# Performance work log

Measured on AMD Instinct MI355X. Metric: run time of the kernel, lower is better.

## Reference

```python
import jax, jax.numpy as jnp
import numpy as np

N = 10000
E = 320000
DIM_IN, DIM_H, DIM_OUT, HEADS = 256, 64, 32, 8
NEG_SLOPE = 0.2


def setup_inputs() -> dict:
    key = jax.random.key(0)
    ks = jax.random.split(key, 10)
    x = jax.random.normal(ks[0], (N, DIM_IN), dtype=jnp.float32)
    edge_index = jax.random.randint(ks[1], (2, E), 0, N, dtype=jnp.int64)
    def glorot(k, shape, fan_in):
        return jax.random.normal(k, shape, dtype=jnp.float32) / np.sqrt(fan_in)
    # layer 1: GATv2Conv(256 -> 64, heads=8)
    W1l = glorot(ks[2], (DIM_IN, HEADS * DIM_H), DIM_IN)
    W1r = glorot(ks[3], (DIM_IN, HEADS * DIM_H), DIM_IN)
    att1 = glorot(ks[4], (HEADS, DIM_H), DIM_H)
    b1 = jnp.zeros((HEADS * DIM_H,), dtype=jnp.float32)
    # layer 2: GATv2Conv(512 -> 32, heads=1)
    W2l = glorot(ks[5], (HEADS * DIM_H, DIM_OUT), HEADS * DIM_H)
    W2r = glorot(ks[6], (HEADS * DIM_H, DIM_OUT), HEADS * DIM_H)
    att2 = glorot(ks[7], (1, DIM_OUT), DIM_OUT)
    b2 = jnp.zeros((DIM_OUT,), dtype=jnp.float32)
    return {"x": x, "edge_index": edge_index, "W1l": W1l, "W1r": W1r,
            "att1": att1, "b1": b1, "W2l": W2l, "W2r": W2r, "att2": att2, "b2": b2}


def gatv2_conv(x, src, dst, Wl, Wr, att, bias, heads, out_ch, concat):
    n = x.shape[0]
    xl = (x @ Wl).reshape(n, heads, out_ch)  # source transform
    xr = (x @ Wr).reshape(n, heads, out_ch)  # target transform
    e = jax.nn.leaky_relu(xl[src] + xr[dst], NEG_SLOPE)       # [E,H,C]
    alpha = jnp.einsum('ehc,hc->eh', e, att)                  # [E,H]
    amax = jax.lax.stop_gradient(
        jax.ops.segment_max(alpha, dst, num_segments=n))      # [N,H]
    ex = jnp.exp(alpha - amax[dst])
    denom = jax.ops.segment_sum(ex, dst, num_segments=n)
    alpha = ex / (denom[dst] + 1e-16)
    msg = xl[src] * alpha[..., None]                          # [E,H,C]
    out = jax.ops.segment_sum(msg, dst, num_segments=n)       # [N,H,C]
    out = out.reshape(n, heads * out_ch) if concat else out.mean(axis=1)
    return out + bias


def reference(x, edge_index, W1l, W1r, att1, b1, W2l, W2r, att2, b2):
    n = x.shape[0]
    loops = jnp.arange(n, dtype=edge_index.dtype)
    src = jnp.concatenate([edge_index[0], loops])  # add_self_loops=True (PyG default)
    dst = jnp.concatenate([edge_index[1], loops])
    h = gatv2_conv(x, src, dst, W1l, W1r, att1, b1, HEADS, DIM_H, True)
    h = jax.nn.elu(h)
    h = gatv2_conv(h, src, dst, W2l, W2r, att2, b2, 1, DIM_OUT, True)
    return jax.nn.log_softmax(h, axis=1)
```

## Files before the change

kernel.cpp:

```cpp
#include <hip/hip_runtime.h>
#include <hip/hip_bf16.h>


constexpr int N_NODES = 10000;
constexpr int N_EDGES = 320000;
constexpr int ET      = N_EDGES + N_NODES;
constexpr float NEG_SLOPE = 0.2f;

constexpr int NB_COUNT  = (ET + 255) / 256;
constexpr int NB_CONVX  = (N_NODES * 64) / 256;
constexpr int NB_CONVW  = (1024 * 64) / 256;
constexpr int NB_CONVW2 = (64 * 128) / 256;
constexpr int NB_M1     = 79 * 8;

typedef __attribute__((ext_vector_type(8))) short short8;
typedef __attribute__((ext_vector_type(8))) unsigned short ushort8_t;
typedef __attribute__((ext_vector_type(4))) float floatx4;
typedef __attribute__((ext_vector_type(2))) float floatx2;

__device__ __forceinline__ float lrelu(float a) {
    return fmaxf(a, NEG_SLOPE * a);
}
__device__ __forceinline__ unsigned short f2bf(float f) {
    unsigned u = __float_as_uint(f);
    unsigned r = u + 0x7FFFu + ((u >> 16) & 1u);
    return (unsigned short)(r >> 16);
}
__device__ __forceinline__ float bf2f(unsigned short h) {
    return __uint_as_float((unsigned)h << 16);
}
__device__ __forceinline__ floatx2 pk_add(floatx2 a, floatx2 b) {
    floatx2 d;
    asm("v_pk_add_f32 %0, %1, %2" : "=v"(d) : "v"(a), "v"(b));
    return d;
}
__device__ __forceinline__ floatx2 pk_fma(floatx2 a, floatx2 b, floatx2 c) {
    floatx2 d;
    asm("v_pk_fma_f32 %0, %1, %2, %3" : "=v"(d) : "v"(a), "v"(b), "v"(c));
    return d;
}
__device__ __forceinline__ floatx2 unpk(unsigned w) {
    floatx2 r;
    r.x = __uint_as_float(w << 16);
    r.y = __uint_as_float(w & 0xffff0000u);
    return r;
}
__device__ __forceinline__ float red8_dpp(float p) {
    int x;
    x = __builtin_amdgcn_update_dpp(0, __float_as_int(p), 0xB1, 0xF, 0xF, true);
    p += __int_as_float(x);
    x = __builtin_amdgcn_update_dpp(0, __float_as_int(p), 0x4E, 0xF, 0xF, true);
    p += __int_as_float(x);
    x = __builtin_amdgcn_update_dpp(0, __float_as_int(p), 0x141, 0xF, 0xF, true);
    p += __int_as_float(x);
    return p;
}
__device__ __forceinline__ float red8max_dpp(float p) {
    int x;
    x = __builtin_amdgcn_update_dpp(0, __float_as_int(p), 0xB1, 0xF, 0xF, true);
    p = fmaxf(p, __int_as_float(x));
    x = __builtin_amdgcn_update_dpp(0, __float_as_int(p), 0x4E, 0xF, 0xF, true);
    p = fmaxf(p, __int_as_float(x));
    x = __builtin_amdgcn_update_dpp(0, __float_as_int(p), 0x141, 0xF, 0xF, true);
    p = fmaxf(p, __int_as_float(x));
    return p;
}
__device__ __forceinline__ float ror8_add(float p) {
    int x = __builtin_amdgcn_update_dpp(0, __float_as_int(p), 0x128, 0xF, 0xF, true);
    return p + __int_as_float(x);
}


__global__ __launch_bounds__(256) void k_prep(const int* __restrict__ ei,
        int* __restrict__ deg, const float* __restrict__ x,
        unsigned short* __restrict__ A, const float* __restrict__ Wl,
        const float* __restrict__ Wr, unsigned short* __restrict__ Bt,
        const float* __restrict__ W2l, const float* __restrict__ W2r,
        unsigned short* __restrict__ Bt2) {
    int b = blockIdx.x, t = threadIdx.x;
    if (b < NB_COUNT) {
        int e = b * 256 + t;
        if (e >= ET) return;
        int d = (e < N_EDGES) ? ei[N_EDGES + e] : (e - N_EDGES);
        atomicAdd(&deg[d], 1);
    } else if (b < NB_COUNT + NB_CONVX) {
        int idx = (b - NB_COUNT) * 256 + t;
        int m = idx >> 6, kg = (idx & 63) << 2;
        float4 v = *reinterpret_cast<const float4*>(x + (size_t)m * 256 + kg);
        ushort4 hi = make_ushort4(f2bf(v.x), f2bf(v.y), f2bf(v.z), f2bf(v.w));
        *reinterpret_cast<ushort4*>(A + (size_t)m * 256 + kg) = hi;
    } else if (b < NB_COUNT + NB_CONVX + NB_CONVW) {
        int idx = (b - NB_COUNT - NB_CONVX) * 256 + t;
        int n = idx >> 6, kg = (idx & 63) << 2;
        const float* src = (n < 512) ? (Wl + n) : (Wr + (n - 512));
        float v0 = src[(size_t)(kg + 0) * 512];
        float v1 = src[(size_t)(kg + 1) * 512];
        float v2 = src[(size_t)(kg + 2) * 512];
        float v3 = src[(size_t)(kg + 3) * 512];
        ushort4 hi = make_ushort4(f2bf(v0), f2bf(v1), f2bf(v2), f2bf(v3));
        *reinterpret_cast<ushort4*>(Bt + (size_t)n * 256 + kg) = hi;
    } else {
        int idx = (b - NB_COUNT - NB_CONVX - NB_CONVW) * 256 + t;
        int j = idx >> 7, kg = (idx & 127) << 2;
        const float* src = (j < 32) ? (W2l + j) : (W2r + (j - 32));
        float v0 = src[(size_t)(kg + 0) * 32];
        float v1 = src[(size_t)(kg + 1) * 32];
        float v2 = src[(size_t)(kg + 2) * 32];
        float v3 = src[(size_t)(kg + 3) * 32];
        ushort4 hi = make_ushort4(f2bf(v0), f2bf(v1), f2bf(v2), f2bf(v3));
        *reinterpret_cast<ushort4*>(Bt2 + (size_t)j * 512 + kg) = hi;
    }
}


__global__ __launch_bounds__(1024) void k_scan(const int* __restrict__ deg,
                                               int* __restrict__ offs) {
    __shared__ int part[1024];
    const int CH = 10;
    int t = threadIdx.x;
    int base = t * CH;
    int loc[CH];
    int s = 0;
    for (int i = 0; i < CH; ++i) {
        int idx = base + i;
        int v = (idx < N_NODES) ? deg[idx] : 0;
        loc[i] = s; s += v;
    }
    part[t] = s;
    __syncthreads();
    for (int o = 1; o < 1024; o <<= 1) {
        int add = (t >= o) ? part[t - o] : 0;
        __syncthreads();
        part[t] += add;
        __syncthreads();
    }
    int excl = part[t] - s;
    for (int i = 0; i < CH; ++i) {
        int idx = base + i;
        if (idx < N_NODES) offs[idx] = excl + loc[i];
    }
    if (t == 1023) offs[N_NODES] = part[1023];
}


__global__ __launch_bounds__(256) void k_scm1(const int* __restrict__ ei,
        const int* __restrict__ offs, int* __restrict__ deg,
        int* __restrict__ ssrc, const unsigned short* __restrict__ A,
        const unsigned short* __restrict__ Bt, unsigned short* __restrict__ xl1b,
        unsigned short* __restrict__ xr1b) {
    __shared__ unsigned short As[128 * 40];
    __shared__ unsigned short Bs[128 * 40];
    int t = threadIdx.x;
    if (blockIdx.x < NB_COUNT) {
        int e = blockIdx.x * 256 + t;
        if (e >= ET) return;
        int s, d;
        if (e < N_EDGES) { s = ei[e]; d = ei[N_EDGES + e]; }
        else             { s = d = e - N_EDGES; }
        int pos = offs[d] + atomicAdd(&deg[d], -1) - 1;
        ssrc[pos] = s;
        return;
    }
    int bb = blockIdx.x - NB_COUNT;
    int row0 = (bb % 79) * 128, n0 = (bb / 79) * 128;
    int wave = t >> 6, L = t & 63;
    int wm = wave & 1, wn = wave >> 1;
    int q = L >> 4, rr = L & 15;
    floatx4 acc[4][4];
#pragma unroll
    for (int i = 0; i < 4; ++i)
#pragma unroll
        for (int j = 0; j < 4; ++j) acc[i][j] = (floatx4){0.f, 0.f, 0.f, 0.f};
    int ra = t >> 2,        ka = (t & 3) * 8;
    int rb = (t + 256) >> 2, kb = ((t + 256) & 3) * 8;
    int gma = row0 + ra; gma = (gma < N_NODES) ? gma : (N_NODES - 1);
    int gmb = row0 + rb; gmb = (gmb < N_NODES) ? gmb : (N_NODES - 1);
    for (int kc = 0; kc < 256; kc += 32) {
        __syncthreads();
        *reinterpret_cast<uint4*>(&As[ra * 40 + ka]) =
            *reinterpret_cast<const uint4*>(A + (size_t)gma * 256 + kc + ka);
        *reinterpret_cast<uint4*>(&As[rb * 40 + kb]) =
            *reinterpret_cast<const uint4*>(A + (size_t)gmb * 256 + kc + kb);
        *reinterpret_cast<uint4*>(&Bs[ra * 40 + ka]) =
            *reinterpret_cast<const uint4*>(Bt + (size_t)(n0 + ra) * 256 + kc + ka);
        *reinterpret_cast<uint4*>(&Bs[rb * 40 + kb]) =
            *reinterpret_cast<const uint4*>(Bt + (size_t)(n0 + rb) * 256 + kc + kb);
        __syncthreads();
        short8 af[4], bf[4];
#pragma unroll
        for (int st = 0; st < 4; ++st)
            af[st] = *reinterpret_cast<const short8*>(
                &As[(wm * 64 + st * 16 + rr) * 40 + q * 8]);
#pragma unroll
        for (int st = 0; st < 4; ++st)
            bf[st] = *reinterpret_cast<const short8*>(
                &Bs[(wn * 64 + st * 16 + rr) * 40 + q * 8]);
#pragma unroll
        for (int i = 0; i < 4; ++i)
#pragma unroll
            for (int j = 0; j < 4; ++j)
                acc[i][j] = __builtin_amdgcn_mfma_f32_16x16x32_bf16(
                    af[i], bf[j], acc[i][j], 0, 0, 0);
    }
#pragma unroll
    for (int j = 0; j < 4; ++j) {
        int gc = n0 + wn * 64 + j * 16 + rr;
        unsigned short* dst = (gc < 512) ? xl1b : xr1b;
        int col = (gc < 512) ? gc : (gc - 512);
#pragma unroll
        for (int i = 0; i < 4; ++i)
#pragma unroll
            for (int r = 0; r < 4; ++r) {
                int gr = row0 + wm * 64 + i * 16 + q * 4 + r;
                if (gr < N_NODES)
                    dst[(size_t)gr * 512 + col] = f2bf(acc[i][j][r]);
            }
    }
}

__global__ __launch_bounds__(256) void k_node1f(const int* __restrict__ offs,
        const int* __restrict__ ssrc, const unsigned short* __restrict__ xl1b,
        const unsigned short* __restrict__ xr1b, const float* __restrict__ att1,
        const float* __restrict__ b1, unsigned short* __restrict__ h1b) {
    __shared__ float comb[2][64][9];
    int t = threadIdx.x;
    int wave = t >> 6, lane = t & 63;
    int ni = wave >> 1, wv = wave & 1;
    int n = blockIdx.x * 2 + ni;
    int beg0 = offs[n], d = offs[n + 1] - beg0;
    int half = (d + 1) >> 1;
    int beg = beg0 + (wv ? half : 0);
    int dcnt = wv ? (d - half) : half;
    floatx2 xrp0, xrp1, xrp2, xrp3;
    floatx2 c1p0, c1p1, c1p2, c1p3;
    floatx2 c2p0, c2p1, c2p2, c2p3;
    float K0;
    {
        ushort8_t xru = *reinterpret_cast<const ushort8_t*>(
            xr1b + (size_t)n * 512 + lane * 8);
        union { ushort8_t v; uint4 w; } cv; cv.v = xru;
        xrp0 = unpk(cv.w.x); xrp1 = unpk(cv.w.y);
        xrp2 = unpk(cv.w.z); xrp3 = unpk(cv.w.w);
        const float* atrow = att1 + lane * 8;
        float4 c0 = *reinterpret_cast<const float4*>(atrow);
        float4 c1 = *reinterpret_cast<const float4*>(atrow + 4);
        c1p0 = (floatx2){0.6f * c0.x, 0.6f * c0.y};
        c1p1 = (floatx2){0.6f * c0.z, 0.6f * c0.w};
        c1p2 = (floatx2){0.6f * c1.x, 0.6f * c1.y};
        c1p3 = (floatx2){0.6f * c1.z, 0.6f * c1.w};
        c2p0 = (floatx2){0.4f * c0.x, 0.4f * c0.y};
        c2p1 = (floatx2){0.4f * c0.z, 0.4f * c0.w};
        c2p2 = (floatx2){0.4f * c1.x, 0.4f * c1.y};
        c2p3 = (floatx2){0.4f * c1.z, 0.4f * c1.w};
        K0 = c1p0.x * xrp0.x + c1p0.y * xrp0.y
           + c1p1.x * xrp1.x + c1p1.y * xrp1.y
           + c1p2.x * xrp2.x + c1p2.y * xrp2.y
           + c1p3.x * xrp3.x + c1p3.y * xrp3.y;
    }
    floatx2 k0p = (floatx2){K0, 0.f};
    float l = 0.f;
    floatx2 ac0 = {0.f, 0.f}, ac1 = {0.f, 0.f}, ac2 = {0.f, 0.f}, ac3 = {0.f, 0.f};
    const int* sp = ssrc + beg;
    const char* xlbase = reinterpret_cast<const char*>(xl1b) + lane * 16;
    auto ld_row = [&](int off) -> ushort8_t {
        return *reinterpret_cast<const ushort8_t*>(xlbase + off);
    };
    for (int b0 = 0; b0 < dcnt; b0 += 64) {
        int bn = dcnt - b0; if (bn > 64) bn = 64;
        int idxv = sp[b0 + ((lane < bn) ? lane : (bn - 1))];
        auto off_at = [&](int k) -> int {
            int kc = (k < bn) ? k : (bn - 1);
            return __shfl(idxv, kc, 64) << 10;
        };
        auto edge = [&](ushort8_t u, int idx) {
            union { ushort8_t v; uint4 w; } cv; cv.v = u;
            floatx2 xs0 = unpk(cv.w.x), xs1 = unpk(cv.w.y),
                    xs2 = unpk(cv.w.z), xs3 = unpk(cv.w.w);
            floatx2 dd = pk_fma(xs0, c1p0, k0p);
            dd = pk_fma(xs1, c1p1, dd);
            dd = pk_fma(xs2, c1p2, dd);
            dd = pk_fma(xs3, c1p3, dd);
            floatx2 a0 = pk_add(xs0, xrp0);
            floatx2 a1 = pk_add(xs1, xrp1);
            floatx2 a2 = pk_add(xs2, xrp2);
            floatx2 a3 = pk_add(xs3, xrp3);
            a0.x = fabsf(a0.x); a0.y = fabsf(a0.y);
            a1.x = fabsf(a1.x); a1.y = fabsf(a1.y);
            a2.x = fabsf(a2.x); a2.y = fabsf(a2.y);
            a3.x = fabsf(a3.x); a3.y = fabsf(a3.y);
            dd = pk_fma(a0, c2p0, dd);
            dd = pk_fma(a1, c2p1, dd);
            dd = pk_fma(a2, c2p2, dd);
            dd = pk_fma(a3, c2p3, dd);
            float p = red8_dpp(dd.x + dd.y);
            float w = __expf(fminf(p, 60.f));
            if (idx >= bn) w = 0.f;
            l += w;
            floatx2 wp = (floatx2){w, w};
            ac0 = pk_fma(xs0, wp, ac0);
            ac1 = pk_fma(xs1, wp, ac1);
            ac2 = pk_fma(xs2, wp, ac2);
            ac3 = pk_fma(xs3, wp, ac3);
        };
        ushort8_t u0 = ld_row(off_at(0));
        ushort8_t u1 = ld_row(off_at(1));
        ushort8_t u2 = ld_row(off_at(2));
        ushort8_t u3 = ld_row(off_at(3));
        for (int i = 0; i < bn; i += 4) {
            ushort8_t p0 = ld_row(off_at(i + 4));
            ushort8_t p1 = ld_row(off_at(i + 5));
            ushort8_t p2 = ld_row(off_at(i + 6));
            ushort8_t p3 = ld_row(off_at(i + 7));
            edge(u0, i);
            edge(u1, i + 1);
            edge(u2, i + 2);
            edge(u3, i + 3);
            u0 = p0; u1 = p1; u2 = p2; u3 = p3;
        }
    }
    if (wv == 1) {
        float* cb = &comb[ni][lane][0];
        cb[0] = ac0.x; cb[1] = ac0.y; cb[2] = ac1.x; cb[3] = ac1.y;
        cb[4] = ac2.x; cb[5] = ac2.y; cb[6] = ac3.x; cb[7] = ac3.y;
        cb[8] = l;
    }
    __syncthreads();
    if (wv == 0) {
        const float* cb = &comb[ni][lane][0];
        float av0 = ac0.x + cb[0], av1 = ac0.y + cb[1];
        float av2 = ac1.x + cb[2], av3 = ac1.y + cb[3];
        float av4 = ac2.x + cb[4], av5 = ac2.y + cb[5];
        float av6 = ac3.x + cb[6], av7 = ac3.y + cb[7];
        float lt = l + cb[8];
        float inv = 1.f / (lt + 1e-16f);
        const float* brow = b1 + lane * 8;
        float av[8] = {av0, av1, av2, av3, av4, av5, av6, av7};
        ushort8_t vout;
#pragma unroll
        for (int j = 0; j < 8; ++j) {
            float v = av[j] * inv + brow[j];
            v = (v > 0.f) ? v : (__expf(v) - 1.f);
            vout[j] = f2bf(v);
        }
        *reinterpret_cast<ushort8_t*>(h1b + (size_t)n * 512 + lane * 8) = vout;
    }
}


__global__ __launch_bounds__(256) void k_mfma2(const unsigned short* __restrict__ h1b,
        const unsigned short* __restrict__ Bt2, float* __restrict__ xw2) {
    __shared__ unsigned short Hs[64 * 40];
    __shared__ unsigned short Ws[64 * 40];
    int t = threadIdx.x;
    int wave = t >> 6, L = t & 63;
    int row0 = blockIdx.x * 64;
    int q = L >> 4, rr = L & 15;
    floatx4 acc[4];
#pragma unroll
    for (int j = 0; j < 4; ++j) acc[j] = (floatx4){0.f, 0.f, 0.f, 0.f};
    int ra = t >> 2, ka = (t & 3) * 8;
    int gma = row0 + ra; gma = (gma < N_NODES) ? gma : (N_NODES - 1);
    for (int kc = 0; kc < 512; kc += 32) {
        __syncthreads();
        *reinterpret_cast<uint4*>(&Hs[ra * 40 + ka]) =
            *reinterpret_cast<const uint4*>(h1b + (size_t)gma * 512 + kc + ka);
        *reinterpret_cast<uint4*>(&Ws[ra * 40 + ka]) =
            *reinterpret_cast<const uint4*>(Bt2 + (size_t)ra * 512 + kc + ka);
        __syncthreads();
        short8 af = *reinterpret_cast<const short8*>(
            &Hs[(wave * 16 + rr) * 40 + q * 8]);
#pragma unroll
        for (int j = 0; j < 4; ++j) {
            short8 bf = *reinterpret_cast<const short8*>(
                &Ws[(j * 16 + rr) * 40 + q * 8]);
            acc[j] = __builtin_amdgcn_mfma_f32_16x16x32_bf16(af, bf, acc[j], 0, 0, 0);
        }
    }
#pragma unroll
    for (int j = 0; j < 4; ++j) {
        int gc = j * 16 + rr;
#pragma unroll
        for (int r = 0; r < 4; ++r) {
            int gr = row0 + wave * 16 + q * 4 + r;
            if (gr < N_NODES) xw2[(size_t)gr * 64 + gc] = acc[j][r];
        }
    }
}

__global__ __launch_bounds__(256) void k_node2f(const int* __restrict__ offs,
        const int* __restrict__ ssrc, const float* __restrict__ xw2,
        const float* __restrict__ att2, const float* __restrict__ b2,
        float* __restrict__ out) {
    int t = threadIdx.x;
    int wave = t >> 6, lane = t & 63;
    int n = blockIdx.x * 4 + wave;
    if (n >= N_NODES) return;
    int ej = lane >> 3;
    int cg = lane & 7;
    int beg = offs[n], dcnt = offs[n + 1] - beg;
    float4 xr = *reinterpret_cast<const float4*>(
                    xw2 + (size_t)n * 64 + 32 + cg * 4);
    float4 at = *reinterpret_cast<const float4*>(att2 + cg * 4);
    float l = 0.f;
    float4 ac = {0.f, 0.f, 0.f, 0.f};
    const int* sp = ssrc + beg;
    const char* xwbase = reinterpret_cast<const char*>(xw2) + cg * 16;
    auto ld_row = [&](int off) -> float4 {
        return *reinterpret_cast<const float4*>(xwbase + off);
    };
    for (int b0 = 0; b0 < dcnt; b0 += 64) {
        int bn = dcnt - b0; if (bn > 64) bn = 64;
        int idxv = sp[b0 + ((lane < bn) ? lane : (bn - 1))];
        auto off_at = [&](int k) -> int {
            int kc = (k < bn) ? k : (bn - 1);
            return __shfl(idxv, kc, 64) << 8;
        };
        float4 uA  = ld_row(off_at(ej));
        float4 uB  = ld_row(off_at(8 + ej));
        float4 uA1 = ld_row(off_at(16 + ej));
        float4 uB1 = ld_row(off_at(24 + ej));
        for (int base = 0; base < bn; base += 16) {
            float4 uA2 = ld_row(off_at(base + 32 + ej));
            float4 uB2 = ld_row(off_at(base + 40 + ej));
            float pA0 = lrelu(uA.x + xr.x) * at.x + lrelu(uA.z + xr.z) * at.z;
            float pA1 = lrelu(uA.y + xr.y) * at.y + lrelu(uA.w + xr.w) * at.w;
            float pB0 = lrelu(uB.x + xr.x) * at.x + lrelu(uB.z + xr.z) * at.z;
            float pB1 = lrelu(uB.y + xr.y) * at.y + lrelu(uB.w + xr.w) * at.w;
            float pA = red8_dpp(pA0 + pA1);
            float pB = red8_dpp(pB0 + pB1);
            if (base + ej >= bn)     pA = -1e30f;
            if (base + 8 + ej >= bn) pB = -1e30f;
            float wA = __expf(fminf(pA, 60.f));
            float wB = __expf(fminf(pB, 60.f));
            l += wA + wB;
            ac.x += wA * uA.x + wB * uB.x;
            ac.y += wA * uA.y + wB * uB.y;
            ac.z += wA * uA.z + wB * uB.z;
            ac.w += wA * uA.w + wB * uB.w;
            uA = uA1; uB = uB1; uA1 = uA2; uB1 = uB2;
        }
    }
    l = ror8_add(l); l += __shfl_xor(l, 16); l += __shfl_xor(l, 32);
    ac.x = ror8_add(ac.x); ac.x += __shfl_xor(ac.x, 16); ac.x += __shfl_xor(ac.x, 32);
    ac.y = ror8_add(ac.y); ac.y += __shfl_xor(ac.y, 16); ac.y += __shfl_xor(ac.y, 32);
    ac.z = ror8_add(ac.z); ac.z += __shfl_xor(ac.z, 16); ac.z += __shfl_xor(ac.z, 32);
    ac.w = ror8_add(ac.w); ac.w += __shfl_xor(ac.w, 16); ac.w += __shfl_xor(ac.w, 32);
    float inv = 1.f / (l + 1e-16f);
    float4 bb = *reinterpret_cast<const float4*>(b2 + cg * 4);
    float4 v;
    v.x = ac.x * inv + bb.x; v.y = ac.y * inv + bb.y;
    v.z = ac.z * inv + bb.z; v.w = ac.w * inv + bb.w;
    float mx = red8max_dpp(fmaxf(fmaxf(v.x, v.y), fmaxf(v.z, v.w)));
    float se = red8_dpp(__expf(v.x - mx) + __expf(v.y - mx)
                      + __expf(v.z - mx) + __expf(v.w - mx));
    float ls = __logf(se);
    v.x = v.x - mx - ls; v.y = v.y - mx - ls;
    v.z = v.z - mx - ls; v.w = v.w - mx - ls;
    if (ej == 0)
        *reinterpret_cast<float4*>(out + (size_t)n * 32 + cg * 4) = v;
}


extern "C" void kernel_launch(void* const* d_in, const int* in_sizes, int n_in,
                              void* d_out, int out_size, void* d_ws, size_t ws_size,
                              hipStream_t stream) {
    (void)in_sizes; (void)n_in; (void)out_size; (void)ws_size;
    const float* x    = (const float*)d_in[0];
    const int*   ei   = (const int*)d_in[1];
    const float* W1l  = (const float*)d_in[2];
    const float* W1r  = (const float*)d_in[3];
    const float* att1 = (const float*)d_in[4];
    const float* b1   = (const float*)d_in[5];
    const float* W2l  = (const float*)d_in[6];
    const float* W2r  = (const float*)d_in[7];
    const float* att2 = (const float*)d_in[8];
    const float* b2   = (const float*)d_in[9];
    float* outp = (float*)d_out;

    char* ws = (char*)d_ws;
    size_t o = 0;
    auto alloc = [&](size_t bytes) {
        char* p = ws + o;
        o = (o + bytes + 255) & ~(size_t)255;
        return p;
    };
    unsigned short* xl1b = (unsigned short*)alloc((size_t)N_NODES * 512 * 2);
    unsigned short* xr1b = (unsigned short*)alloc((size_t)N_NODES * 512 * 2);
    unsigned short* h1b  = (unsigned short*)alloc((size_t)N_NODES * 512 * 2);
    float* xw2    = (float*)alloc((size_t)N_NODES * 64 * 4);
    unsigned short* Abf = (unsigned short*)alloc((size_t)N_NODES * 256 * 2);
    unsigned short* Bbf = (unsigned short*)alloc((size_t)1024 * 256 * 2);
    unsigned short* Bt2 = (unsigned short*)alloc((size_t)64 * 512 * 2);
    int*   deg    = (int*)alloc((size_t)N_NODES * 4);
    int*   offs   = (int*)alloc((size_t)(N_NODES + 1) * 4);
    int*   ssrc   = (int*)alloc((size_t)ET * 4);

    hipMemsetAsync(deg, 0, (size_t)N_NODES * 4, stream);

    k_prep   <<<NB_COUNT + NB_CONVX + NB_CONVW + NB_CONVW2, 256, 0, stream>>>(
                 ei, deg, x, Abf, W1l, W1r, Bbf, W2l, W2r, Bt2);
    k_scan   <<<1,                    1024, 0, stream>>>(deg, offs);
    k_scm1   <<<NB_COUNT + NB_M1,      256, 0, stream>>>(ei, offs, deg, ssrc,
                                                         Abf, Bbf, xl1b, xr1b);
    k_node1f <<<N_NODES / 2,           256, 0, stream>>>(offs, ssrc, xl1b, xr1b, att1, b1, h1b);
    k_mfma2  <<<(N_NODES + 63) / 64,   256, 0, stream>>>(h1b, Bt2, xw2);
    k_node2f <<<(N_NODES + 3) / 4,     256, 0, stream>>>(offs, ssrc, xw2, att2, b2, outp);
}
```

Before: 201.9 us.

## Assign one wave per node in layer-1 aggregation with deeper prefetch

Each wave now processes a whole node's edge list alone, so two waves no longer split a node and merge partial sums through shared memory with a block barrier. To keep enough gathers in flight, the edge loop is unrolled to eight rows with two prefetch groups. A launch-bounds occupancy hint is also added. This removes the LDS merge and __syncthreads, but each wave's serial chain doubles in length and the larger register footprint could reduce occupancy.

```diff
diff --git a/kernel.cpp b/kernel.cpp
--- a/kernel.cpp
+++ b/kernel.cpp
@@ -218,19 +218,15 @@
     }
 }
 
-__global__ __launch_bounds__(256) void k_node1f(const int* __restrict__ offs,
+__global__ __launch_bounds__(256, 4) void k_node1f(const int* __restrict__ offs,
         const int* __restrict__ ssrc, const unsigned short* __restrict__ xl1b,
         const unsigned short* __restrict__ xr1b, const float* __restrict__ att1,
         const float* __restrict__ b1, unsigned short* __restrict__ h1b) {
-    __shared__ float comb[2][64][9];
     int t = threadIdx.x;
     int wave = t >> 6, lane = t & 63;
-    int ni = wave >> 1, wv = wave & 1;
-    int n = blockIdx.x * 2 + ni;
-    int beg0 = offs[n], d = offs[n + 1] - beg0;
-    int half = (d + 1) >> 1;
-    int beg = beg0 + (wv ? half : 0);
-    int dcnt = wv ? (d - half) : half;
+    int n = blockIdx.x * 4 + wave;
+    if (n >= N_NODES) return;
+    int beg = offs[n], dcnt = offs[n + 1] - beg;
     floatx2 xrp0, xrp1, xrp2, xrp3;
     floatx2 c1p0, c1p1, c1p2, c1p3;
     floatx2 c2p0, c2p1, c2p2, c2p3;
@@ -302,48 +298,46 @@
             ac2 = pk_fma(xs2, wp, ac2);
             ac3 = pk_fma(xs3, wp, ac3);
         };
-        ushort8_t u0 = ld_row(off_at(0));
-        ushort8_t u1 = ld_row(off_at(1));
-        ushort8_t u2 = ld_row(off_at(2));
-        ushort8_t u3 = ld_row(off_at(3));
-        for (int i = 0; i < bn; i += 4) {
-            ushort8_t p0 = ld_row(off_at(i + 4));
-            ushort8_t p1 = ld_row(off_at(i + 5));
-            ushort8_t p2 = ld_row(off_at(i + 6));
-            ushort8_t p3 = ld_row(off_at(i + 7));
-            edge(u0, i);
-            edge(u1, i + 1);
-            edge(u2, i + 2);
-            edge(u3, i + 3);
-            u0 = p0; u1 = p1; u2 = p2; u3 = p3;
+        ushort8_t uA0 = ld_row(off_at(0));
+        ushort8_t uA1 = ld_row(off_at(1));
+        ushort8_t uA2 = ld_row(off_at(2));
+        ushort8_t uA3 = ld_row(off_at(3));
+        ushort8_t uB0 = ld_row(off_at(4));
+        ushort8_t uB1 = ld_row(off_at(5));
+        ushort8_t uB2 = ld_row(off_at(6));
+        ushort8_t uB3 = ld_row(off_at(7));
+        for (int i = 0; i < bn; i += 8) {
+            ushort8_t pA0 = ld_row(off_at(i + 8));
+            ushort8_t pA1 = ld_row(off_at(i + 9));
+            ushort8_t pA2 = ld_row(off_at(i + 10));
+            ushort8_t pA3 = ld_row(off_at(i + 11));
+            edge(uA0, i);
+            edge(uA1, i + 1);
+            edge(uA2, i + 2);
+            edge(uA3, i + 3);
+            ushort8_t pB0 = ld_row(off_at(i + 12));
+            ushort8_t pB1 = ld_row(off_at(i + 13));
+            ushort8_t pB2 = ld_row(off_at(i + 14));
+            ushort8_t pB3 = ld_row(off_at(i + 15));
+            edge(uB0, i + 4);
+            edge(uB1, i + 5);
+            edge(uB2, i + 6);
+            edge(uB3, i + 7);
+            uA0 = pA0; uA1 = pA1; uA2 = pA2; uA3 = pA3;
+            uB0 = pB0; uB1 = pB1; uB2 = pB2; uB3 = pB3;
         }
     }
-    if (wv == 1) {
-        float* cb = &comb[ni][lane][0];
-        cb[0] = ac0.x; cb[1] = ac0.y; cb[2] = ac1.x; cb[3] = ac1.y;
-        cb[4] = ac2.x; cb[5] = ac2.y; cb[6] = ac3.x; cb[7] = ac3.y;
-        cb[8] = l;
-    }
-    __syncthreads();
-    if (wv == 0) {
-        const float* cb = &comb[ni][lane][0];
-        float av0 = ac0.x + cb[0], av1 = ac0.y + cb[1];
-        float av2 = ac1.x + cb[2], av3 = ac1.y + cb[3];
-        float av4 = ac2.x + cb[4], av5 = ac2.y + cb[5];
-        float av6 = ac3.x + cb[6], av7 = ac3.y + cb[7];
-        float lt = l + cb[8];
-        float inv = 1.f / (lt + 1e-16f);
-        const float* brow = b1 + lane * 8;
-        float av[8] = {av0, av1, av2, av3, av4, av5, av6, av7};
-        ushort8_t vout;
-#pragma unroll
-        for (int j = 0; j < 8; ++j) {
-            float v = av[j] * inv + brow[j];
-            v = (v > 0.f) ? v : (__expf(v) - 1.f);
-            vout[j] = f2bf(v);
-        }
-        *reinterpret_cast<ushort8_t*>(h1b + (size_t)n * 512 + lane * 8) = vout;
-    }
+    float inv = 1.f / (l + 1e-16f);
+    const float* brow = b1 + lane * 8;
+    float av[8] = {ac0.x, ac0.y, ac1.x, ac1.y, ac2.x, ac2.y, ac3.x, ac3.y};
+    ushort8_t vout;
+#pragma unroll
+    for (int j = 0; j < 8; ++j) {
+        float v = av[j] * inv + brow[j];
+        v = (v > 0.f) ? v : (__expf(v) - 1.f);
+        vout[j] = f2bf(v);
+    }
+    *reinterpret_cast<ushort8_t*>(h1b + (size_t)n * 512 + lane * 8) = vout;
 }
 
 
@@ -502,7 +496,7 @@
     k_scan   <<<1,                    1024, 0, stream>>>(deg, offs);
     k_scm1   <<<NB_COUNT + NB_M1,      256, 0, stream>>>(ei, offs, deg, ssrc,
                                                          Abf, Bbf, xl1b, xr1b);
-    k_node1f <<<N_NODES / 2,           256, 0, stream>>>(offs, ssrc, xl1b, xr1b, att1, b1, h1b);
+    k_node1f <<<(N_NODES + 3) / 4,     256, 0, stream>>>(offs, ssrc, xl1b, xr1b, att1, b1, h1b);
     k_mfma2  <<<(N_NODES + 63) / 64,   256, 0, stream>>>(h1b, Bt2, xw2);
     k_node2f <<<(N_NODES + 3) / 4,     256, 0, stream>>>(offs, ssrc, xw2, att2, b2, outp);
 }
```

New measurement: 202.0 us. About the same (+0.1%).
